# Performance work log

Hardware: AMD Instinct MI355X
Metric: run time of the kernel (lower is better)

## Reference

```python
import jax, jax.numpy as jnp
import numpy as np

N = 50000
E = 800000
D_IN = 64
D_OUT = 64
D_EDGE = 16


def setup_inputs() -> dict:
    key = jax.random.key(0)
    ks = jax.random.split(key, 10)
    x = jax.random.normal(ks[0], (N, D_IN), dtype=jnp.float32)
    edge_index = jax.random.randint(ks[1], (2, E), 0, N, dtype=jnp.int64)
    edge_attr = jax.random.normal(ks[2], (E, D_EDGE), dtype=jnp.float32)
    s = 1.0 / np.sqrt(D_EDGE)
    We = jax.random.uniform(ks[3], (D_EDGE, D_IN), minval=-s, maxval=s, dtype=jnp.float32)
    be = jax.random.uniform(ks[4], (D_IN,), minval=-s, maxval=s, dtype=jnp.float32)
    s1 = 1.0 / np.sqrt(D_IN)
    W1 = jax.random.uniform(ks[5], (D_IN, D_OUT), minval=-s1, maxval=s1, dtype=jnp.float32)
    b1 = jax.random.uniform(ks[6], (D_OUT,), minval=-s1, maxval=s1, dtype=jnp.float32)
    s2 = 1.0 / np.sqrt(D_OUT)
    W2 = jax.random.uniform(ks[7], (D_OUT, D_OUT), minval=-s2, maxval=s2, dtype=jnp.float32)
    b2 = jax.random.uniform(ks[8], (D_OUT,), minval=-s2, maxval=s2, dtype=jnp.float32)
    return {"x": x, "edge_index": edge_index, "edge_attr": edge_attr,
            "We": We, "be": be, "W1": W1, "b1": b1, "W2": W2, "b2": b2}


def reference(x, edge_index, edge_attr, We, be, W1, b1, W2, b2):
    src = edge_index[0]  # message source j
    dst = edge_index[1]  # aggregation target i (PyG source_to_target flow)
    # per-edge message: relu(x_j + lin_edge(edge_attr))
    msg = jax.nn.relu(x[src] + edge_attr @ We + be)  # [E, D_IN]
    # scatter-sum aggregation at target nodes
    agg = jax.ops.segment_sum(msg, dst, num_segments=N)  # [N, D_IN]
    eps = 0.0  # GINEConv default, train_eps=False
    h = (1.0 + eps) * x + agg
    # mlp: Linear -> ReLU -> Linear (dropout p=0.0 -> identity)
    out = jax.nn.relu(h @ W1 + b1) @ W2 + b2
    return out
```

## Files before the change

kernel.cpp:

```cpp
#include <hip/hip_runtime.h>
#include <hip/hip_fp16.h>
#include <hip/hip_bf16.h>

#define NN 50000
#define EE 800000
#define NSLICE 8
#define SLICE 6250
#define NCHUNK 256
#define CHUNK 3125
#define WQ 784

#define OFF_AGGH 0ull
#define OFF_SD   6400000ull
#define OFF_FLAG 12800000ull

__device__ __forceinline__ float bflo(unsigned u) { return __uint_as_float(u << 16); }
__device__ __forceinline__ float bfhi(unsigned u) { return __uint_as_float(u & 0xffff0000u); }

__global__ void detect_dtype(const unsigned* __restrict__ xw, int* __restrict__ flag) {
    const int t = threadIdx.x;
    unsigned e = (xw[t] >> 7) & 0xFFu;
    unsigned long long m = __ballot(e >= 100u && e <= 140u);
    if (t == 0) *flag = (__popcll(m) >= 32) ? 1 : 0;
}

__global__ __launch_bounds__(256) void pack_kernel(const int* __restrict__ ei,
                                                   unsigned* __restrict__ sd) {
    const int oddor = ei[1] | ei[3] | ei[5] | ei[7] | ei[9] | ei[11] | ei[13] | ei[15];
    const bool idx64 = (oddor == 0);
    const long long* __restrict__ ei64 = (const long long*)ei;
    const int e = blockIdx.x * 256 + threadIdx.x;
    int src, dst;
    if (idx64) { src = (int)ei64[e]; dst = (int)ei64[EE + e]; }
    else       { src = ei[e];        dst = ei[EE + e]; }
    sd[e] = (unsigned)src | ((unsigned)dst << 16);
}

template <bool BF16>
__device__ __forceinline__ float edge_lin(const void* __restrict__ eav, int e,
                                          const float* __restrict__ we, float bed) {
    float acc = bed;
    if constexpr (BF16) {
        const uint4* row = (const uint4*)((const __hip_bfloat16*)eav + (size_t)e * 16);
        const uint4 p0 = row[0];
        const uint4 p1 = row[1];
        acc = fmaf(bflo(p0.x), we[0],  acc); acc = fmaf(bfhi(p0.x), we[1],  acc);
        acc = fmaf(bflo(p0.y), we[2],  acc); acc = fmaf(bfhi(p0.y), we[3],  acc);
        acc = fmaf(bflo(p0.z), we[4],  acc); acc = fmaf(bfhi(p0.z), we[5],  acc);
        acc = fmaf(bflo(p0.w), we[6],  acc); acc = fmaf(bfhi(p0.w), we[7],  acc);
        acc = fmaf(bflo(p1.x), we[8],  acc); acc = fmaf(bfhi(p1.x), we[9],  acc);
        acc = fmaf(bflo(p1.y), we[10], acc); acc = fmaf(bfhi(p1.y), we[11], acc);
        acc = fmaf(bflo(p1.z), we[12], acc); acc = fmaf(bfhi(p1.z), we[13], acc);
        acc = fmaf(bflo(p1.w), we[14], acc); acc = fmaf(bfhi(p1.w), we[15], acc);
    } else {
        const float4* row = (const float4*)((const float*)eav + (size_t)e * 16);
        const float4 q0 = row[0], q1 = row[1], q2 = row[2], q3 = row[3];
        acc = fmaf(q0.x, we[0],  acc); acc = fmaf(q0.y, we[1],  acc);
        acc = fmaf(q0.z, we[2],  acc); acc = fmaf(q0.w, we[3],  acc);
        acc = fmaf(q1.x, we[4],  acc); acc = fmaf(q1.y, we[5],  acc);
        acc = fmaf(q1.z, we[6],  acc); acc = fmaf(q1.w, we[7],  acc);
        acc = fmaf(q2.x, we[8],  acc); acc = fmaf(q2.y, we[9],  acc);
        acc = fmaf(q2.z, we[10], acc); acc = fmaf(q2.w, we[11], acc);
        acc = fmaf(q3.x, we[12], acc); acc = fmaf(q3.y, we[13], acc);
        acc = fmaf(q3.z, we[14], acc); acc = fmaf(q3.w, we[15], acc);
    }
    return acc;
}

template <bool BF16>
__device__ __forceinline__ float loadx(const void* __restrict__ xv, int s, int d) {
    if constexpr (BF16)
        return __bfloat162float(((const __hip_bfloat16*)xv)[(size_t)s * 64 + d]);
    else
        return ((const float*)xv)[(size_t)s * 64 + d];
}

template <bool BF16>
__device__ __forceinline__ void do_edge(
    const void* __restrict__ xv, const void* __restrict__ eav,
    const float* __restrict__ we, float bed, __half2* __restrict__ aggh,
    int src, int dst, int eid, int d)
{
    const float xs  = loadx<BF16>(xv, src, d);
    const float a   = edge_lin<BF16>(eav, eid, we, bed);
    const float msg = fmaxf(a + xs, 0.0f);
    const float oth = __shfl_xor(msg, 1);
    if ((d & 1) == 0) {
        __half2 v = __floats2half2_rn(msg, oth);
        unsafeAtomicAdd(aggh + (size_t)dst * 32 + (d >> 1), v);
    }
}

template <bool BF16>
__device__ __forceinline__ void slice_body(
    const void* __restrict__ xv, const unsigned* __restrict__ sd,
    const void* __restrict__ eav, const void* __restrict__ Wev,
    const void* __restrict__ bev, __half2* __restrict__ aggh,
    uint2 (*q)[WQ])
{
    const int tid  = threadIdx.x;
    const int d    = tid & 63;
    const int sub  = tid >> 6;
    const int p    = blockIdx.x & 7;
    const int c    = blockIdx.x >> 3;

    float we[16];
    float bed;
    if constexpr (BF16) {
        const __hip_bfloat16* We = (const __hip_bfloat16*)Wev;
#pragma unroll
        for (int k = 0; k < 16; k++) we[k] = __bfloat162float(We[k * 64 + d]);
        bed = __bfloat162float(((const __hip_bfloat16*)bev)[d]);
    } else {
        const float* We = (const float*)Wev;
#pragma unroll
        for (int k = 0; k < 16; k++) we[k] = We[k * 64 + d];
        bed = ((const float*)bev)[d];
    }

    const int cb = c * CHUNK;
    const int a0 = cb + sub * 782;
    const int a1 = cb + min(CHUNK, (sub + 1) * 782);

    int cnt = 0;
    for (int base = a0; base < a1; base += 64) {
        const int e = base + d;
        unsigned v = 0;
        bool own = false;
        if (e < a1) {
            v = sd[e];
            own = ((int)(v & 0xFFFFu) / SLICE) == p;
        }
        const unsigned long long m = __ballot(own);
        if (own) {
            const int rank = __popcll(m & ((1ull << d) - 1ull));
            q[sub][cnt + rank] = make_uint2(v, (unsigned)e);
        }
        cnt += __popcll(m);
    }

    int k = 0;
    for (; k + 4 <= cnt; k += 4) {
        const uint2 r0 = q[sub][k],     r1 = q[sub][k + 1];
        const uint2 r2 = q[sub][k + 2], r3 = q[sub][k + 3];
        const int s0 = r0.x & 0xFFFFu, t0 = r0.x >> 16, e0 = (int)r0.y;
        const int s1 = r1.x & 0xFFFFu, t1 = r1.x >> 16, e1 = (int)r1.y;
        const int s2 = r2.x & 0xFFFFu, t2 = r2.x >> 16, e2 = (int)r2.y;
        const int s3 = r3.x & 0xFFFFu, t3 = r3.x >> 16, e3 = (int)r3.y;
        const float x0 = loadx<BF16>(xv, s0, d);
        const float x1 = loadx<BF16>(xv, s1, d);
        const float x2 = loadx<BF16>(xv, s2, d);
        const float x3 = loadx<BF16>(xv, s3, d);
        const float a0f = edge_lin<BF16>(eav, e0, we, bed);
        const float a1f = edge_lin<BF16>(eav, e1, we, bed);
        const float a2f = edge_lin<BF16>(eav, e2, we, bed);
        const float a3f = edge_lin<BF16>(eav, e3, we, bed);
        const float m0 = fmaxf(a0f + x0, 0.0f);
        const float m1 = fmaxf(a1f + x1, 0.0f);
        const float m2 = fmaxf(a2f + x2, 0.0f);
        const float m3 = fmaxf(a3f + x3, 0.0f);
        const float o0 = __shfl_xor(m0, 1);
        const float o1 = __shfl_xor(m1, 1);
        const float o2 = __shfl_xor(m2, 1);
        const float o3 = __shfl_xor(m3, 1);
        if ((d & 1) == 0) {
            const int h = d >> 1;
            unsafeAtomicAdd(aggh + (size_t)t0 * 32 + h, __floats2half2_rn(m0, o0));
            unsafeAtomicAdd(aggh + (size_t)t1 * 32 + h, __floats2half2_rn(m1, o1));
            unsafeAtomicAdd(aggh + (size_t)t2 * 32 + h, __floats2half2_rn(m2, o2));
            unsafeAtomicAdd(aggh + (size_t)t3 * 32 + h, __floats2half2_rn(m3, o3));
        }
    }
    for (; k < cnt; ++k) {
        const uint2 r = q[sub][k];
        do_edge<BF16>(xv, eav, we, bed, aggh,
                      (int)(r.x & 0xFFFFu), (int)(r.x >> 16), (int)r.y, d);
    }
}

__global__ __launch_bounds__(256) void slice_agg_kernel(
    const void* x, const unsigned* sd, const void* ea,
    const void* We, const void* be, __half2* aggh, const int* flag)
{
    __shared__ uint2 q[4][WQ];
    if (*flag) slice_body<true >(x, sd, ea, We, be, aggh, q);
    else       slice_body<false>(x, sd, ea, We, be, aggh, q);
}

template <bool BF16>
__device__ __forceinline__ void mlp_body(
    const void* __restrict__ xv, const __half* __restrict__ aggh,
    const void* __restrict__ W1v, const void* __restrict__ b1v,
    const void* __restrict__ W2v, const void* __restrict__ b2v,
    void* __restrict__ outv, float (*sh)[64], float (*st)[64])
{
    const int tid = threadIdx.x;
    const int d   = tid & 63;
    const int w   = tid >> 6;

    float w1c[64], w2c[64], b1d, b2d;
    if constexpr (BF16) {
        const __hip_bfloat16* W1 = (const __hip_bfloat16*)W1v;
        const __hip_bfloat16* W2 = (const __hip_bfloat16*)W2v;
#pragma unroll
        for (int k = 0; k < 64; k++) {
            w1c[k] = __bfloat162float(W1[k * 64 + d]);
            w2c[k] = __bfloat162float(W2[k * 64 + d]);
        }
        b1d = __bfloat162float(((const __hip_bfloat16*)b1v)[d]);
        b2d = __bfloat162float(((const __hip_bfloat16*)b2v)[d]);
    } else {
        const float* W1 = (const float*)W1v;
        const float* W2 = (const float*)W2v;
#pragma unroll
        for (int k = 0; k < 64; k++) {
            w1c[k] = W1[k * 64 + d];
            w2c[k] = W2[k * 64 + d];
        }
        b1d = ((const float*)b1v)[d];
        b2d = ((const float*)b2v)[d];
    }

    const int stride = gridDim.x * 4;
    int node = blockIdx.x * 4 + w;

    float xs_n = 0.0f, ag_n = 0.0f;
    if (node < NN) {
        if constexpr (BF16) xs_n = __bfloat162float(((const __hip_bfloat16*)xv)[(size_t)node * 64 + d]);
        else                xs_n = ((const float*)xv)[(size_t)node * 64 + d];
        ag_n = __half2float(aggh[(size_t)node * 64 + d]);
    }

    while (node < NN) {
        const float xs_c = xs_n, ag_c = ag_n;
        const int next = node + stride;
        if (next < NN) {
            if constexpr (BF16) xs_n = __bfloat162float(((const __hip_bfloat16*)xv)[(size_t)next * 64 + d]);
            else                xs_n = ((const float*)xv)[(size_t)next * 64 + d];
            ag_n = __half2float(aggh[(size_t)next * 64 + d]);
        }

        sh[w][d] = xs_c + ag_c;

        float t = b1d;
        const float4* hv = (const float4*)sh[w];
#pragma unroll
        for (int k = 0; k < 16; k++) {
            const float4 hq = hv[k];
            t = fmaf(hq.x, w1c[4 * k],     t);
            t = fmaf(hq.y, w1c[4 * k + 1], t);
            t = fmaf(hq.z, w1c[4 * k + 2], t);
            t = fmaf(hq.w, w1c[4 * k + 3], t);
        }
        t = fmaxf(t, 0.0f);
        st[w][d] = t;

        float o = b2d;
        const float4* tv = (const float4*)st[w];
#pragma unroll
        for (int k = 0; k < 16; k++) {
            const float4 tq = tv[k];
            o = fmaf(tq.x, w2c[4 * k],     o);
            o = fmaf(tq.y, w2c[4 * k + 1], o);
            o = fmaf(tq.z, w2c[4 * k + 2], o);
            o = fmaf(tq.w, w2c[4 * k + 3], o);
        }
        if constexpr (BF16) ((__hip_bfloat16*)outv)[(size_t)node * 64 + d] = __float2bfloat16(o);
        else                ((float*)outv)[(size_t)node * 64 + d] = o;
        node = next;
    }
}

__global__ __launch_bounds__(256) void mlp_kernel(
    const void* x, const __half* aggh,
    const void* W1, const void* b1, const void* W2, const void* b2,
    void* out, const int* flag)
{
    __shared__ float sh[4][64];
    __shared__ float st[4][64];
    if (*flag) mlp_body<true >(x, aggh, W1, b1, W2, b2, out, sh, st);
    else       mlp_body<false>(x, aggh, W1, b1, W2, b2, out, sh, st);
}

extern "C" void kernel_launch(void* const* d_in, const int* in_sizes, int n_in,
                              void* d_out, int out_size, void* d_ws, size_t ws_size,
                              hipStream_t stream) {
    const void* x          = d_in[0];
    const int*  edge_index = (const int*)d_in[1];
    const void* edge_attr  = d_in[2];
    const void* We         = d_in[3];
    const void* be         = d_in[4];
    const void* W1         = d_in[5];
    const void* b1         = d_in[6];
    const void* W2         = d_in[7];
    const void* b2         = d_in[8];

    char* ws = (char*)d_ws;
    __half*   aggh = (__half*)(ws + OFF_AGGH);
    unsigned* sd   = (unsigned*)(ws + OFF_SD);
    int*      flag = (int*)(ws + OFF_FLAG);

    hipMemsetAsync(aggh, 0, (size_t)NN * 64 * sizeof(__half), stream);
    hipLaunchKernelGGL(detect_dtype, dim3(1), dim3(64), 0, stream,
                       (const unsigned*)x, flag);
    hipLaunchKernelGGL(pack_kernel, dim3(EE / 256), dim3(256), 0, stream,
                       edge_index, sd);
    hipLaunchKernelGGL(slice_agg_kernel, dim3(NSLICE * NCHUNK), dim3(256), 0, stream,
                       x, sd, edge_attr, We, be, (__half2*)aggh, flag);
    hipLaunchKernelGGL(mlp_kernel, dim3(768), dim3(256), 0, stream,
                       x, aggh, W1, b1, W2, b2, d_out, flag);
}
```

Baseline: 275.4 us.

## Replace per-block slice filtering with global counting sort of edges by source slice

Drops the packed-edge pass and the per-block ballot filtering, where every slice block rescanned its chunk of edges. In their place, a histogram kernel (which also does dtype detection) and a binning kernel bucket edge records by source slice. The records go into the output buffer as scratch, so each aggregation wave reads a contiguous range of its own edges. The cost is a second pass over edge_index, plus shared and global atomics on only eight counters. The MLP dot products also switch to four independent accumulators to shorten the FMA dependency chain.

```diff
diff --git a/kernel.cpp b/kernel.cpp
--- a/kernel.cpp
+++ b/kernel.cpp
@@ -6,34 +6,70 @@
 #define EE 800000
 #define NSLICE 8
 #define SLICE 6250
-#define NCHUNK 256
-#define CHUNK 3125
-#define WQ 784
+#define EBLK 3125
 
 #define OFF_AGGH 0ull
-#define OFF_SD   6400000ull
+#define OFF_CNT  6400000ull
+#define OFF_CUR  6400032ull
 #define OFF_FLAG 12800000ull
 
 __device__ __forceinline__ float bflo(unsigned u) { return __uint_as_float(u << 16); }
 __device__ __forceinline__ float bfhi(unsigned u) { return __uint_as_float(u & 0xffff0000u); }
 
-__global__ void detect_dtype(const unsigned* __restrict__ xw, int* __restrict__ flag) {
-    const int t = threadIdx.x;
-    unsigned e = (xw[t] >> 7) & 0xFFu;
-    unsigned long long m = __ballot(e >= 100u && e <= 140u);
-    if (t == 0) *flag = (__popcll(m) >= 32) ? 1 : 0;
-}
-
-__global__ __launch_bounds__(256) void pack_kernel(const int* __restrict__ ei,
-                                                   unsigned* __restrict__ sd) {
+__device__ __forceinline__ void load_edge(const int* __restrict__ ei, bool idx64, int e,
+                                          int& src, int& dst) {
+    const long long* __restrict__ ei64 = (const long long*)ei;
+    if (idx64) { src = (int)ei64[e]; dst = (int)ei64[EE + e]; }
+    else       { src = ei[e];        dst = ei[EE + e]; }
+}
+
+__global__ __launch_bounds__(256) void hist_detect_kernel(const int* __restrict__ ei,
+                                                          const unsigned* __restrict__ xw,
+                                                          int* __restrict__ cnt8,
+                                                          int* __restrict__ flag) {
+    __shared__ int h[8];
+    const int tid = threadIdx.x;
+    if (tid < 8) h[tid] = 0;
+    __syncthreads();
     const int oddor = ei[1] | ei[3] | ei[5] | ei[7] | ei[9] | ei[11] | ei[13] | ei[15];
     const bool idx64 = (oddor == 0);
-    const long long* __restrict__ ei64 = (const long long*)ei;
-    const int e = blockIdx.x * 256 + threadIdx.x;
     int src, dst;
-    if (idx64) { src = (int)ei64[e]; dst = (int)ei64[EE + e]; }
-    else       { src = ei[e];        dst = ei[EE + e]; }
-    sd[e] = (unsigned)src | ((unsigned)dst << 16);
+    load_edge(ei, idx64, blockIdx.x * 256 + tid, src, dst);
+    atomicAdd(&h[src / SLICE], 1);
+    __syncthreads();
+    if (tid < 8) atomicAdd(&cnt8[tid], h[tid]);
+    if (blockIdx.x == 0 && tid < 64) {
+        unsigned ex = (xw[tid] >> 7) & 0xFFu;
+        unsigned long long m = __ballot(ex >= 100u && ex <= 140u);
+        if (tid == 0) *flag = (__popcll(m) >= 32) ? 1 : 0;
+    }
+}
+
+__global__ __launch_bounds__(256) void bin_kernel(const int* __restrict__ ei,
+                                                  const int* __restrict__ cnt8,
+                                                  int* __restrict__ cur8,
+                                                  uint2* __restrict__ recs) {
+    __shared__ int lcnt[8], gb[8], pre[8];
+    const int tid = threadIdx.x;
+    if (tid < 8) lcnt[tid] = 0;
+    __syncthreads();
+    const int oddor = ei[1] | ei[3] | ei[5] | ei[7] | ei[9] | ei[11] | ei[13] | ei[15];
+    const bool idx64 = (oddor == 0);
+    const int e = blockIdx.x * 256 + tid;
+    int src, dst;
+    load_edge(ei, idx64, e, src, dst);
+    const int p = src / SLICE;
+    const int lrank = atomicAdd(&lcnt[p], 1);
+    __syncthreads();
+    if (tid < 8) {
+        gb[tid] = atomicAdd(&cur8[tid], lcnt[tid]);
+        int s = 0;
+        for (int i = 0; i < tid; i++) s += cnt8[i];
+        pre[tid] = s;
+    }
+    __syncthreads();
+    recs[pre[p] + gb[p] + lrank] =
+        make_uint2((unsigned)src | ((unsigned)dst << 16), (unsigned)e);
 }
 
 template <bool BF16>
@@ -76,33 +112,17 @@
 }
 
 template <bool BF16>
-__device__ __forceinline__ void do_edge(
-    const void* __restrict__ xv, const void* __restrict__ eav,
-    const float* __restrict__ we, float bed, __half2* __restrict__ aggh,
-    int src, int dst, int eid, int d)
+__device__ __forceinline__ void slice_body(
+    const void* __restrict__ xv, const uint2* __restrict__ recs,
+    const int* __restrict__ cnt8,
+    const void* __restrict__ eav, const void* __restrict__ Wev,
+    const void* __restrict__ bev, __half2* __restrict__ aggh)
 {
-    const float xs  = loadx<BF16>(xv, src, d);
-    const float a   = edge_lin<BF16>(eav, eid, we, bed);
-    const float msg = fmaxf(a + xs, 0.0f);
-    const float oth = __shfl_xor(msg, 1);
-    if ((d & 1) == 0) {
-        __half2 v = __floats2half2_rn(msg, oth);
-        unsafeAtomicAdd(aggh + (size_t)dst * 32 + (d >> 1), v);
-    }
-}
-
-template <bool BF16>
-__device__ __forceinline__ void slice_body(
-    const void* __restrict__ xv, const unsigned* __restrict__ sd,
-    const void* __restrict__ eav, const void* __restrict__ Wev,
-    const void* __restrict__ bev, __half2* __restrict__ aggh,
-    uint2 (*q)[WQ])
-{
-    const int tid  = threadIdx.x;
-    const int d    = tid & 63;
-    const int sub  = tid >> 6;
-    const int p    = blockIdx.x & 7;
-    const int c    = blockIdx.x >> 3;
+    const int tid = threadIdx.x;
+    const int d   = tid & 63;
+    const int sub = tid >> 6;
+    const int p   = blockIdx.x & 7;
+    const int c   = blockIdx.x >> 3;
 
     float we[16];
     float bed;
@@ -118,31 +138,19 @@
         bed = ((const float*)bev)[d];
     }
 
-    const int cb = c * CHUNK;
-    const int a0 = cb + sub * 782;
-    const int a1 = cb + min(CHUNK, (sub + 1) * 782);
-
-    int cnt = 0;
-    for (int base = a0; base < a1; base += 64) {
-        const int e = base + d;
-        unsigned v = 0;
-        bool own = false;
-        if (e < a1) {
-            v = sd[e];
-            own = ((int)(v & 0xFFFFu) / SLICE) == p;
-        }
-        const unsigned long long m = __ballot(own);
-        if (own) {
-            const int rank = __popcll(m & ((1ull << d) - 1ull));
-            q[sub][cnt + rank] = make_uint2(v, (unsigned)e);
-        }
-        cnt += __popcll(m);
-    }
-
-    int k = 0;
-    for (; k + 4 <= cnt; k += 4) {
-        const uint2 r0 = q[sub][k],     r1 = q[sub][k + 1];
-        const uint2 r2 = q[sub][k + 2], r3 = q[sub][k + 3];
+    int B = 0;
+#pragma unroll
+    for (int i = 0; i < 8; i++) B += (i < p) ? cnt8[i] : 0;
+    const int C = cnt8[p];
+    const int lo = B + (int)((long long)C * c / 256);
+    const int hi = B + (int)((long long)C * (c + 1) / 256);
+    const int w0 = lo + (int)((long long)(hi - lo) * sub / 4);
+    const int w1 = lo + (int)((long long)(hi - lo) * (sub + 1) / 4);
+
+    int k = w0;
+    for (; k + 4 <= w1; k += 4) {
+        const uint2 r0 = recs[k],     r1 = recs[k + 1];
+        const uint2 r2 = recs[k + 2], r3 = recs[k + 3];
         const int s0 = r0.x & 0xFFFFu, t0 = r0.x >> 16, e0 = (int)r0.y;
         const int s1 = r1.x & 0xFFFFu, t1 = r1.x >> 16, e1 = (int)r1.y;
         const int s2 = r2.x & 0xFFFFu, t2 = r2.x >> 16, e2 = (int)r2.y;
@@ -171,20 +179,24 @@
             unsafeAtomicAdd(aggh + (size_t)t3 * 32 + h, __floats2half2_rn(m3, o3));
         }
     }
-    for (; k < cnt; ++k) {
-        const uint2 r = q[sub][k];
-        do_edge<BF16>(xv, eav, we, bed, aggh,
-                      (int)(r.x & 0xFFFFu), (int)(r.x >> 16), (int)r.y, d);
+    for (; k < w1; ++k) {
+        const uint2 r = recs[k];
+        const int s0 = r.x & 0xFFFFu, t0 = r.x >> 16, e0 = (int)r.y;
+        const float xs  = loadx<BF16>(xv, s0, d);
+        const float a   = edge_lin<BF16>(eav, e0, we, bed);
+        const float msg = fmaxf(a + xs, 0.0f);
+        const float oth = __shfl_xor(msg, 1);
+        if ((d & 1) == 0)
+            unsafeAtomicAdd(aggh + (size_t)t0 * 32 + (d >> 1), __floats2half2_rn(msg, oth));
     }
 }
 
 __global__ __launch_bounds__(256) void slice_agg_kernel(
-    const void* x, const unsigned* sd, const void* ea,
+    const void* x, const uint2* recs, const int* cnt8, const void* ea,
     const void* We, const void* be, __half2* aggh, const int* flag)
 {
-    __shared__ uint2 q[4][WQ];
-    if (*flag) slice_body<true >(x, sd, ea, We, be, aggh, q);
-    else       slice_body<false>(x, sd, ea, We, be, aggh, q);
+    if (*flag) slice_body<true >(x, recs, cnt8, ea, We, be, aggh);
+    else       slice_body<false>(x, recs, cnt8, ea, We, be, aggh);
 }
 
 template <bool BF16>
@@ -242,29 +254,30 @@
 
         sh[w][d] = xs_c + ag_c;
 
-        float t = b1d;
+        float t0 = 0.0f, t1 = 0.0f, t2 = 0.0f, t3 = 0.0f;
         const float4* hv = (const float4*)sh[w];
 #pragma unroll
         for (int k = 0; k < 16; k++) {
             const float4 hq = hv[k];
-            t = fmaf(hq.x, w1c[4 * k],     t);
-            t = fmaf(hq.y, w1c[4 * k + 1], t);
-            t = fmaf(hq.z, w1c[4 * k + 2], t);
-            t = fmaf(hq.w, w1c[4 * k + 3], t);
-        }
-        t = fmaxf(t, 0.0f);
+            t0 = fmaf(hq.x, w1c[4 * k],     t0);
+            t1 = fmaf(hq.y, w1c[4 * k + 1], t1);
+            t2 = fmaf(hq.z, w1c[4 * k + 2], t2);
+            t3 = fmaf(hq.w, w1c[4 * k + 3], t3);
+        }
+        const float t = fmaxf(b1d + ((t0 + t1) + (t2 + t3)), 0.0f);
         st[w][d] = t;
 
-        float o = b2d;
+        float o0 = 0.0f, o1 = 0.0f, o2 = 0.0f, o3 = 0.0f;
         const float4* tv = (const float4*)st[w];
 #pragma unroll
         for (int k = 0; k < 16; k++) {
             const float4 tq = tv[k];
-            o = fmaf(tq.x, w2c[4 * k],     o);
-            o = fmaf(tq.y, w2c[4 * k + 1], o);
-            o = fmaf(tq.z, w2c[4 * k + 2], o);
-            o = fmaf(tq.w, w2c[4 * k + 3], o);
-        }
+            o0 = fmaf(tq.x, w2c[4 * k],     o0);
+            o1 = fmaf(tq.y, w2c[4 * k + 1], o1);
+            o2 = fmaf(tq.z, w2c[4 * k + 2], o2);
+            o3 = fmaf(tq.w, w2c[4 * k + 3], o3);
+        }
+        const float o = b2d + ((o0 + o1) + (o2 + o3));
         if constexpr (BF16) ((__hip_bfloat16*)outv)[(size_t)node * 64 + d] = __float2bfloat16(o);
         else                ((float*)outv)[(size_t)node * 64 + d] = o;
         node = next;
@@ -296,17 +309,20 @@
     const void* b2         = d_in[8];
 
     char* ws = (char*)d_ws;
-    __half*   aggh = (__half*)(ws + OFF_AGGH);
-    unsigned* sd   = (unsigned*)(ws + OFF_SD);
-    int*      flag = (int*)(ws + OFF_FLAG);
+    __half* aggh = (__half*)(ws + OFF_AGGH);
+    int*    cnt8 = (int*)(ws + OFF_CNT);
+    int*    cur8 = (int*)(ws + OFF_CUR);
+    int*    flag = (int*)(ws + OFF_FLAG);
+    uint2*  recs = (uint2*)d_out;
 
     hipMemsetAsync(aggh, 0, (size_t)NN * 64 * sizeof(__half), stream);
-    hipLaunchKernelGGL(detect_dtype, dim3(1), dim3(64), 0, stream,
-                       (const unsigned*)x, flag);
-    hipLaunchKernelGGL(pack_kernel, dim3(EE / 256), dim3(256), 0, stream,
-                       edge_index, sd);
-    hipLaunchKernelGGL(slice_agg_kernel, dim3(NSLICE * NCHUNK), dim3(256), 0, stream,
-                       x, sd, edge_attr, We, be, (__half2*)aggh, flag);
+    hipMemsetAsync(cnt8, 0, 64, stream);
+    hipLaunchKernelGGL(hist_detect_kernel, dim3(EBLK), dim3(256), 0, stream,
+                       edge_index, (const unsigned*)x, cnt8, flag);
+    hipLaunchKernelGGL(bin_kernel, dim3(EBLK), dim3(256), 0, stream,
+                       edge_index, cnt8, cur8, recs);
+    hipLaunchKernelGGL(slice_agg_kernel, dim3(NSLICE * 256), dim3(256), 0, stream,
+                       x, recs, cnt8, edge_attr, We, be, (__half2*)aggh, flag);
     hipLaunchKernelGGL(mlp_kernel, dim3(768), dim3(256), 0, stream,
                        x, aggh, W1, b1, W2, b2, d_out, flag);
 }
```

Measured after the change: 359.5 us. +30.5%, slower.
